# Kernel tuning notes

Measured on AMD Instinct MI355X. Metric: run time of the kernel, lower is better.

## Reference

```python
import jax, jax.numpy as jnp
import numpy as np

H = 1024        # hidden_size
NH = 16         # num_attention_heads
DH = H // NH    # head dim = 64
I = 4096        # intermediate_size
E = 8           # moe_num_experts
B, S = 2, 2048
EPS = 1e-12


def _ln(x, g, b):
    mu = jnp.mean(x, axis=-1, keepdims=True)
    var = jnp.mean(jnp.square(x - mu), axis=-1, keepdims=True)
    return (x - mu) * jax.lax.rsqrt(var + EPS) * g + b


def setup_inputs() -> dict:
    key = jax.random.key(0)
    ks = jax.random.split(key, 16)
    std = 0.02
    p = {
        "hidden_states": jax.random.normal(ks[0], (B, S, H), jnp.float32),
        "Wq": jax.random.normal(ks[1], (H, H), jnp.float32) * std,
        "bq": jnp.zeros((H,), jnp.float32),
        "Wk": jax.random.normal(ks[2], (H, H), jnp.float32) * std,
        "bk": jnp.zeros((H,), jnp.float32),
        "Wv": jax.random.normal(ks[3], (H, H), jnp.float32) * std,
        "bv": jnp.zeros((H,), jnp.float32),
        "Wao": jax.random.normal(ks[4], (H, H), jnp.float32) * std,
        "bao": jnp.zeros((H,), jnp.float32),
        "ln1_g": jnp.ones((H,), jnp.float32),
        "ln1_b": jnp.zeros((H,), jnp.float32),
        "router_w": jax.random.normal(ks[5], (H, E), jnp.float32) * std,
        "We": jax.random.normal(ks[6], (E, H, I), jnp.float32) * std,
        "be": jnp.zeros((E, I), jnp.float32),
        "Wo": jax.random.normal(ks[7], (I, H), jnp.float32) * std,
        "bo": jnp.zeros((H,), jnp.float32),
        "ln2_g": jnp.ones((H,), jnp.float32),
        "ln2_b": jnp.zeros((H,), jnp.float32),
    }
    return p


def reference(hidden_states, Wq, bq, Wk, bk, Wv, bv, Wao, bao, ln1_g, ln1_b,
              router_w, We, be, Wo, bo, ln2_g, ln2_b):
    x = hidden_states  # [B,S,H]

    def heads(t):  # [B,S,H] -> [B,NH,S,DH]
        return t.reshape(B, S, NH, DH).transpose(0, 2, 1, 3)

    q = heads(x @ Wq + bq)
    k = heads(x @ Wk + bk)
    v = heads(x @ Wv + bv)
    scores = jnp.einsum("bhqd,bhkd->bhqk", q, k) / jnp.sqrt(jnp.float32(DH))
    probs = jax.nn.softmax(scores, axis=-1)
    ctx = jnp.einsum("bhqk,bhkd->bhqd", probs, v)
    ctx = ctx.transpose(0, 2, 1, 3).reshape(B, S, H)
    attn_out = _ln(ctx @ Wao + bao + x, ln1_g, ln1_b)  # BertSelfOutput

    # ---- MoE FFN: top-1 routing, per-expert GELU MLP, shared output proj ----
    flat = attn_out.reshape(-1, H)              # [N,H]
    logits = flat @ router_w                    # [N,E]
    idx = jnp.argmax(logits, axis=-1)           # top-1 of softmax == argmax of logits
    inter = jnp.zeros((flat.shape[0], I), flat.dtype)
    for e in range(E):  # small fixed expert count
        h_e = jax.nn.gelu(flat @ We[e] + be[e], approximate=False)
        inter = jnp.where((idx == e)[:, None], h_e, inter)
    inter = inter.reshape(B, S, I)
    out = _ln(inter @ Wo + bo + attn_out, ln2_g, ln2_b)  # BertOutput
    return out
```

## Files before the change

### kernel.cpp

```cpp
#include <hip/hip_runtime.h>
#include <hip/hip_bf16.h>
#include <cstdint>

#define H_  1024
#define NH_ 16
#define DH_ 64
#define I_  4096
#define E_  8
#define B_  2
#define S_  2048
#define N_  4096
#define QKVLD 3072
#define LN_EPS 1e-12f

typedef __attribute__((ext_vector_type(4))) float f4;
typedef __attribute__((ext_vector_type(8))) short s8v;
typedef unsigned int u32;

__device__ __forceinline__ float bf2f(unsigned short u) {
  union { unsigned int i; float f; } c; c.i = ((unsigned int)u) << 16; return c.f;
}
__device__ __forceinline__ unsigned short f2bf(float f) {
  __hip_bfloat16 h = __float2bfloat16(f);
  return *reinterpret_cast<unsigned short*>(&h);
}
__device__ __forceinline__ u32 pack_bf2(float a, float b) {
  return (u32)f2bf(a) | ((u32)f2bf(b) << 16);
}
__device__ __forceinline__ float gelu_f(float x) {
  return 0.5f * x * (1.0f + erff(x * 0.70710678118f));
}
__device__ __forceinline__ void gload16(const void* g, void* l) {
  __builtin_amdgcn_global_load_lds(
      (const __attribute__((address_space(1))) void*)g,
      (__attribute__((address_space(3))) void*)l, 16, 0, 0);
}

__global__ __launch_bounds__(256) void cvt_bf16_kernel(
    const float* __restrict__ in, ushort* __restrict__ out, int n8)
{
  const int t = blockIdx.x * 256 + threadIdx.x;
  if (t >= n8) return;
  const f4 x0 = *(const f4*)(in + (size_t)t * 8);
  const f4 x1 = *(const f4*)(in + (size_t)t * 8 + 4);
  s8v o;
#pragma unroll
  for (int j = 0; j < 4; ++j) { o[j] = (short)f2bf(x0[j]); o[4 + j] = (short)f2bf(x1[j]); }
  *(s8v*)(out + (size_t)t * 8) = o;
}

__global__ __launch_bounds__(256) void transpose_cvt_kernel(
    const float* __restrict__ in, ushort* __restrict__ out, int R, int C)
{
  __shared__ float tile[32][33];
  const size_t zo = (size_t)blockIdx.z * R * C;
  const int bx = blockIdx.x << 5, by = blockIdx.y << 5;
  const int tx = threadIdx.x & 31, ty = threadIdx.x >> 5;
  const float* ip = in + zo + (size_t)by * C + bx;
#pragma unroll
  for (int i = 0; i < 4; ++i)
    tile[ty + 8 * i][tx] = ip[(size_t)(ty + 8 * i) * C + tx];
  __syncthreads();
  ushort* op = out + zo + (size_t)bx * R + by;
#pragma unroll
  for (int i = 0; i < 4; ++i)
    op[(size_t)(ty + 8 * i) * R + tx] = f2bf(tile[tx][ty + 8 * i]);
}

__global__ void concat3_kernel(const float* a, const float* b, const float* c,
                               float* __restrict__ o)
{
  const int t = blockIdx.x * 256 + threadIdx.x;
  if (t < 1024) o[t] = a[t];
  else if (t < 2048) o[t] = b[t - 1024];
  else o[t] = c[t - 2048];
}

__global__ __launch_bounds__(256) void gather_kernel(
    const ushort* __restrict__ X, const int* __restrict__ lists,
    ushort* __restrict__ Xg)
{
  const int r = (blockIdx.x << 1) + (threadIdx.x >> 7);
  const int c = (threadIdx.x & 127) << 3;
  const int tok = lists[r];
  *(s8v*)&Xg[(size_t)r * H_ + c] = *(const s8v*)&X[(size_t)tok * H_ + c];
}

template <bool BF16OUT, int KSPLIT>
__global__ __launch_bounds__(256, 4) void gemm_mfma_kernel(
    const ushort* __restrict__ A, const ushort* __restrict__ Bt,
    const float* __restrict__ bias, void* __restrict__ Cout,
    const int M, const int N, const int K)
{
  __shared__ __align__(16) ushort Asm[2][4][128][8];
  __shared__ __align__(16) ushort Bsm[2][4][128][8];
  const int tid = threadIdx.x;
  const int w = tid >> 6, l = tid & 63;
  const int lq = l & 15, g = l >> 4;
  const int wm = w >> 1, wn = w & 1;
  const int nbx = N >> 7;
  const int nwg = nbx * (M >> 7);
  int id = blockIdx.y * nbx + blockIdx.x;
  id = (id & 7) * (nwg >> 3) + (id >> 3);
  const int m0 = (id / nbx) << 7, n0 = (id % nbx) << 7;
  const int Kspan = K / KSPLIT;
  const int kbase = (KSPLIT > 1) ? blockIdx.z * Kspan : 0;

  const ushort* a0 = A + (size_t)(m0 + l) * K + kbase + (w << 3);
  const ushort* a1 = a0 + (size_t)64 * K;
  const ushort* b0 = Bt + (size_t)(n0 + l) * K + kbase + (w << 3);
  const ushort* b1 = b0 + (size_t)64 * K;

  f4 acc[4][4] = {};
  const int nt = Kspan >> 5;
#define STAGE_G(tt, buf)                                   \
  { const int kt_ = (tt) << 5;                             \
    gload16(a0 + kt_, &Asm[buf][w][0][0]);                 \
    gload16(a1 + kt_, &Asm[buf][w][64][0]);                \
    gload16(b0 + kt_, &Bsm[buf][w][0][0]);                 \
    gload16(b1 + kt_, &Bsm[buf][w][64][0]); }
  STAGE_G(0, 0);
  STAGE_G(1, 1);
  for (int t = 0; t < nt; ++t) {
    const int cur = t & 1;
    if (t + 1 < nt) { asm volatile("s_waitcnt vmcnt(4)" ::: "memory"); }
    else            { asm volatile("s_waitcnt vmcnt(0)" ::: "memory"); }
    __builtin_amdgcn_s_barrier();
    __builtin_amdgcn_sched_barrier(0);
    s8v af[4], bfv[4];
#pragma unroll
    for (int mi = 0; mi < 4; ++mi)
      af[mi] = *(const s8v*)&Asm[cur][g][(wm << 6) + (mi << 4) + lq][0];
#pragma unroll
    for (int ni = 0; ni < 4; ++ni)
      bfv[ni] = *(const s8v*)&Bsm[cur][g][(wn << 6) + (ni << 4) + lq][0];
    asm volatile("s_waitcnt lgkmcnt(0)" ::: "memory");
    __builtin_amdgcn_sched_barrier(0);
    __builtin_amdgcn_s_barrier();
    __builtin_amdgcn_sched_barrier(0);
    if (t + 2 < nt) STAGE_G(t + 2, cur);
#pragma unroll
    for (int mi = 0; mi < 4; ++mi)
#pragma unroll
      for (int ni = 0; ni < 4; ++ni)
        acc[mi][ni] = __builtin_amdgcn_mfma_f32_16x16x32_bf16(af[mi], bfv[ni], acc[mi][ni], 0, 0, 0);
  }
#undef STAGE_G
  if constexpr (BF16OUT) {
    ushort* st = (ushort*)Asm + (size_t)w * (16 * 72);
    float bs[4];
#pragma unroll
    for (int ni = 0; ni < 4; ++ni) bs[ni] = bias[n0 + (wn << 6) + (ni << 4) + lq];
#pragma unroll
    for (int mi = 0; mi < 4; ++mi) {
#pragma unroll
      for (int ni = 0; ni < 4; ++ni)
#pragma unroll
        for (int r = 0; r < 4; ++r)
          st[((g << 2) + r) * 72 + (ni << 4) + lq] = f2bf(acc[mi][ni][r] + bs[ni]);
#pragma unroll
      for (int q2 = 0; q2 < 2; ++q2) {
        const int r16 = l & 15, ch = (l >> 4) + (q2 << 2);
        const s8v vv = *(const s8v*)&st[r16 * 72 + (ch << 3)];
        *(s8v*)&((ushort*)Cout)[(size_t)(m0 + (wm << 6) + (mi << 4) + r16) * N
                                + n0 + (wn << 6) + (ch << 3)] = vv;
      }
    }
  } else {
    float* outf = (float*)Cout + (size_t)blockIdx.z * M * N;
#pragma unroll
    for (int ni = 0; ni < 4; ++ni) {
      const int col = n0 + (wn << 6) + (ni << 4) + lq;
      const float bs = (KSPLIT == 1 || blockIdx.z == 0) ? bias[col] : 0.f;
#pragma unroll
      for (int mi = 0; mi < 4; ++mi) {
        const int row = m0 + (wm << 6) + (mi << 4) + (g << 2);
#pragma unroll
        for (int r = 0; r < 4; ++r)
          outf[(size_t)(row + r) * N + col] = acc[mi][ni][r] + bs;
      }
    }
  }
}

__global__ __launch_bounds__(256, 4) void moe_mfma_kernel(
    const ushort* __restrict__ Xg, const ushort* __restrict__ WeT,
    const float* __restrict__ be, const int* __restrict__ lists,
    const int* __restrict__ offs, const int* __restrict__ cnt,
    const int* __restrict__ tb, ushort* __restrict__ inter)
{
  __shared__ __align__(16) ushort Asm[2][4][128][8];
  __shared__ __align__(16) ushort Bsm[2][4][128][8];
  __shared__ int tokL[128];
  const int by = blockIdx.y;
  if (by >= tb[E_]) return;
  int e = 0;
#pragma unroll
  for (int t = 1; t < E_; ++t) if (by >= tb[t]) e = t;
  const int rt = by - tb[e];
  const int base = offs[e] + (rt << 7);
  const int nrows = cnt[e] - (rt << 7);
  const int tid = threadIdx.x;
  if (tid < 128) tokL[tid] = (tid < nrows) ? lists[base + tid] : -1;
  __syncthreads();
  const int w = tid >> 6, l = tid & 63;
  const int lq = l & 15, g = l >> 4;
  const int wm = w >> 1, wn = w & 1;
  const int n0 = blockIdx.x << 7;
  const int r0 = min(base + l, N_ - 1);
  const int r1 = min(base + 64 + l, N_ - 1);
  const ushort* a0 = Xg + (size_t)r0 * H_ + (w << 3);
  const ushort* a1 = Xg + (size_t)r1 * H_ + (w << 3);
  const ushort* Wp = WeT + (size_t)e * I_ * H_;
  const ushort* b0 = Wp + (size_t)(n0 + l) * H_ + (w << 3);
  const ushort* b1 = b0 + (size_t)64 * H_;

  f4 acc[4][4] = {};
#define STAGE_M(tt, buf)                                   \
  { const int kt_ = (tt) << 5;                             \
    gload16(a0 + kt_, &Asm[buf][w][0][0]);                 \
    gload16(a1 + kt_, &Asm[buf][w][64][0]);                \
    gload16(b0 + kt_, &Bsm[buf][w][0][0]);                 \
    gload16(b1 + kt_, &Bsm[buf][w][64][0]); }
  STAGE_M(0, 0);
  STAGE_M(1, 1);
  for (int t = 0; t < 32; ++t) {
    const int cur = t & 1;
    if (t + 1 < 32) { asm volatile("s_waitcnt vmcnt(4)" ::: "memory"); }
    else            { asm volatile("s_waitcnt vmcnt(0)" ::: "memory"); }
    __builtin_amdgcn_s_barrier();
    __builtin_amdgcn_sched_barrier(0);
    s8v af[4], bfv[4];
#pragma unroll
    for (int mi = 0; mi < 4; ++mi)
      af[mi] = *(const s8v*)&Asm[cur][g][(wm << 6) + (mi << 4) + lq][0];
#pragma unroll
    for (int ni = 0; ni < 4; ++ni)
      bfv[ni] = *(const s8v*)&Bsm[cur][g][(wn << 6) + (ni << 4) + lq][0];
    asm volatile("s_waitcnt lgkmcnt(0)" ::: "memory");
    __builtin_amdgcn_sched_barrier(0);
    __builtin_amdgcn_s_barrier();
    __builtin_amdgcn_sched_barrier(0);
    if (t + 2 < 32) STAGE_M(t + 2, cur);
#pragma unroll
    for (int mi = 0; mi < 4; ++mi)
#pragma unroll
      for (int ni = 0; ni < 4; ++ni)
        acc[mi][ni] = __builtin_amdgcn_mfma_f32_16x16x32_bf16(af[mi], bfv[ni], acc[mi][ni], 0, 0, 0);
  }
#undef STAGE_M
  {
    ushort* st = (ushort*)Asm + (size_t)w * (16 * 72);
    float bs[4];
#pragma unroll
    for (int ni = 0; ni < 4; ++ni) bs[ni] = be[(size_t)e * I_ + n0 + (wn << 6) + (ni << 4) + lq];
#pragma unroll
    for (int mi = 0; mi < 4; ++mi) {
#pragma unroll
      for (int ni = 0; ni < 4; ++ni)
#pragma unroll
        for (int r = 0; r < 4; ++r)
          st[((g << 2) + r) * 72 + (ni << 4) + lq] = f2bf(gelu_f(acc[mi][ni][r] + bs[ni]));
#pragma unroll
      for (int q2 = 0; q2 < 2; ++q2) {
        const int r16 = l & 15, ch = (l >> 4) + (q2 << 2);
        const int tok = tokL[(wm << 6) + (mi << 4) + r16];
        if (tok >= 0) {
          const s8v vv = *(const s8v*)&st[r16 * 72 + (ch << 3)];
          *(s8v*)&inter[(size_t)tok * I_ + n0 + (wn << 6) + (ch << 3)] = vv;
        }
      }
    }
  }
}

__global__ __launch_bounds__(256) void attn_mfma_kernel(
    const ushort* __restrict__ qkv, ushort* __restrict__ ctx)
{
  __shared__ __align__(16) ushort Ks[64 * 72];
  __shared__ __align__(16) ushort Vr[64 * 72];
  __shared__ __align__(16) ushort Vt[64 * 72];
  __shared__ __align__(16) ushort Ps[4][16 * 72];
  const int bid0 = blockIdx.x;
  const int bid  = ((bid0 & 7) << 7) + (bid0 >> 3);
  const int bh = bid >> 5, qt = bid & 31;
  const int b = bh >> 4, h = bh & 15;
  const int tid = threadIdx.x, w = tid >> 6, l = tid & 63;
  const int lq = l & 15, g = l >> 4;
  const size_t bS = (size_t)b * S_;
  const ushort* qb = qkv + bS * QKVLD + h * DH_;
  const ushort* kb = qb + 1024;
  const ushort* vb = qb + 2048;

  s8v qf0, qf1;
  {
    const ushort* qp = qb + (size_t)(qt * 64 + w * 16 + lq) * QKVLD;
    qf0 = *(const s8v*)(qp + (g << 3));
    qf1 = *(const s8v*)(qp + 32 + (g << 3));
  }

  f4 o0 = {0,0,0,0}, o1 = {0,0,0,0}, o2 = {0,0,0,0}, o3 = {0,0,0,0};
  float mrun = -3.0e38f, lrun = 0.f;

  const int skey = tid >> 2;
  const int sd   = (tid & 3) << 4;

  s8v kr0, kr1, vr0, vr1;
#define ALOAD(t_) {                                                        \
    const ushort* kp_ = kb + (size_t)((t_) * 64 + skey) * QKVLD + sd;      \
    kr0 = *(const s8v*)kp_; kr1 = *(const s8v*)(kp_ + 8);                  \
    const ushort* vp_ = vb + (size_t)((t_) * 64 + skey) * QKVLD + sd;      \
    vr0 = *(const s8v*)vp_; vr1 = *(const s8v*)(vp_ + 8); }
#define AWRITE() {                                                         \
    *(s8v*)&Ks[skey * 72 + sd]     = kr0;                                  \
    *(s8v*)&Ks[skey * 72 + sd + 8] = kr1;                                  \
    *(s8v*)&Vr[skey * 72 + sd]     = vr0;                                  \
    *(s8v*)&Vr[skey * 72 + sd + 8] = vr1; }

  ALOAD(0); AWRITE();
  ALOAD(1);

  for (int kt = 0; kt < 32; ++kt) {
    asm volatile("s_waitcnt lgkmcnt(0)" ::: "memory");
    __builtin_amdgcn_sched_barrier(0);
    __builtin_amdgcn_s_barrier();
    __builtin_amdgcn_sched_barrier(0);

    {
      s8v t0, t1;
#pragma unroll
      for (int j = 0; j < 8; ++j) {
        t0[j] = (short)Vr[(w * 16 + j) * 72 + l];
        t1[j] = (short)Vr[(w * 16 + 8 + j) * 72 + l];
      }
      *(s8v*)&Vt[l * 72 + w * 16]     = t0;
      *(s8v*)&Vt[l * 72 + w * 16 + 8] = t1;
    }

    float s[16];
    __builtin_amdgcn_s_setprio(1);
#pragma unroll
    for (int st = 0; st < 4; ++st) {
      f4 acc = {0, 0, 0, 0};
      const s8v ka0 = *(const s8v*)&Ks[(st * 16 + lq) * 72 + (g << 3)];
      const s8v ka1 = *(const s8v*)&Ks[(st * 16 + lq) * 72 + 32 + (g << 3)];
      acc = __builtin_amdgcn_mfma_f32_16x16x32_bf16(ka0, qf0, acc, 0, 0, 0);
      acc = __builtin_amdgcn_mfma_f32_16x16x32_bf16(ka1, qf1, acc, 0, 0, 0);
      s[st * 4 + 0] = acc[0] * 0.125f; s[st * 4 + 1] = acc[1] * 0.125f;
      s[st * 4 + 2] = acc[2] * 0.125f; s[st * 4 + 3] = acc[3] * 0.125f;
    }
    __builtin_amdgcn_s_setprio(0);

    float tmax = s[0];
#pragma unroll
    for (int i = 1; i < 16; ++i) tmax = fmaxf(tmax, s[i]);
    tmax = fmaxf(tmax, __shfl_xor(tmax, 16));
    tmax = fmaxf(tmax, __shfl_xor(tmax, 32));
    if (!__all(tmax - mrun <= 8.f)) {
      const float mnew  = fmaxf(mrun, tmax);
      const float alpha = __expf(mrun - mnew);
      f4 av;
      av[0] = __shfl(alpha, g * 4 + 0); av[1] = __shfl(alpha, g * 4 + 1);
      av[2] = __shfl(alpha, g * 4 + 2); av[3] = __shfl(alpha, g * 4 + 3);
      o0 *= av; o1 *= av; o2 *= av; o3 *= av;
      lrun *= alpha; mrun = mnew;
    }
    float psum = 0.f;
#pragma unroll
    for (int i = 0; i < 16; ++i) { s[i] = __expf(s[i] - mrun); psum += s[i]; }
    psum += __shfl_xor(psum, 16); psum += __shfl_xor(psum, 32);
    lrun += psum;

    {
      ushort* pw = &Ps[w][lq * 72];
#pragma unroll
      for (int st = 0; st < 4; ++st) {
        *(u32*)&pw[st * 16 + g * 4 + 0] = pack_bf2(s[st * 4 + 0], s[st * 4 + 1]);
        *(u32*)&pw[st * 16 + g * 4 + 2] = pack_bf2(s[st * 4 + 2], s[st * 4 + 3]);
      }
    }
    asm volatile("s_waitcnt lgkmcnt(0)" ::: "memory");
    __builtin_amdgcn_sched_barrier(0);
    __builtin_amdgcn_s_barrier();
    __builtin_amdgcn_sched_barrier(0);

    __builtin_amdgcn_s_setprio(1);
#pragma unroll
    for (int ks = 0; ks < 2; ++ks) {
      const int kof = ks * 32 + (g << 3);
      const s8v pa = *(const s8v*)&Ps[w][lq * 72 + kof];
      const s8v v0 = *(const s8v*)&Vt[( 0 + lq) * 72 + kof];
      const s8v v1 = *(const s8v*)&Vt[(16 + lq) * 72 + kof];
      const s8v v2 = *(const s8v*)&Vt[(32 + lq) * 72 + kof];
      const s8v v3 = *(const s8v*)&Vt[(48 + lq) * 72 + kof];
      o0 = __builtin_amdgcn_mfma_f32_16x16x32_bf16(pa, v0, o0, 0, 0, 0);
      o1 = __builtin_amdgcn_mfma_f32_16x16x32_bf16(pa, v1, o1, 0, 0, 0);
      o2 = __builtin_amdgcn_mfma_f32_16x16x32_bf16(pa, v2, o2, 0, 0, 0);
      o3 = __builtin_amdgcn_mfma_f32_16x16x32_bf16(pa, v3, o3, 0, 0, 0);
    }
    __builtin_amdgcn_s_setprio(0);

    if (kt + 1 < 32) AWRITE();
    if (kt + 2 < 32) ALOAD(kt + 2);
  }
#undef ALOAD
#undef AWRITE

  const float inv = 1.f / lrun;
#pragma unroll
  for (int r = 0; r < 4; ++r) {
    const float li = __shfl(inv, g * 4 + r);
    ushort* op = ctx + (bS + (size_t)(qt * 64 + w * 16 + g * 4 + r)) * H_ + h * DH_ + lq;
    op[0]  = f2bf(o0[r] * li);
    op[16] = f2bf(o1[r] * li);
    op[32] = f2bf(o2[r] * li);
    op[48] = f2bf(o3[r] * li);
  }
}

template <int P>
__global__ __launch_bounds__(256) void add_ln_kernel(
    const float* __restrict__ a, const float* __restrict__ r,
    const float* __restrict__ g, const float* __restrict__ bta,
    float* __restrict__ out, ushort* __restrict__ ob)
{
  const int row = blockIdx.x, tid = threadIdx.x;
  const size_t base = (size_t)row * H_;
  const float4 xr = *(const float4*)(r + base + (tid << 2));
  float4 x = xr;
#pragma unroll
  for (int pp = 0; pp < P; ++pp) {
    const float4 xa = *(const float4*)(a + (size_t)pp * N_ * H_ + base + (tid << 2));
    x.x += xa.x; x.y += xa.y; x.z += xa.z; x.w += xa.w;
  }
  float s  = x.x + x.y + x.z + x.w;
  float ss = x.x * x.x + x.y * x.y + x.z * x.z + x.w * x.w;
#pragma unroll
  for (int off = 1; off < 64; off <<= 1) { s += __shfl_xor(s, off); ss += __shfl_xor(ss, off); }
  __shared__ float red[8];
  const int w = tid >> 6, ln = tid & 63;
  if (ln == 0) { red[w] = s; red[4 + w] = ss; }
  __syncthreads();
  const float S  = red[0] + red[1] + red[2] + red[3];
  const float SS = red[4] + red[5] + red[6] + red[7];
  const float mu  = S * (1.f / 1024.f);
  const float var = fmaxf(SS * (1.f / 1024.f) - mu * mu, 0.f);
  const float inv = rsqrtf(var + LN_EPS);
  const float4 gg = *(const float4*)&g[tid << 2];
  const float4 bb = *(const float4*)&bta[tid << 2];
  float4 y;
  y.x = (x.x - mu) * inv * gg.x + bb.x;
  y.y = (x.y - mu) * inv * gg.y + bb.y;
  y.z = (x.z - mu) * inv * gg.z + bb.z;
  y.w = (x.w - mu) * inv * gg.w + bb.w;
  *(float4*)&out[base + (tid << 2)] = y;
  if (ob) {
    ushort4 u;
    u.x = f2bf(y.x); u.y = f2bf(y.y); u.z = f2bf(y.z); u.w = f2bf(y.w);
    *(ushort4*)&ob[base + (tid << 2)] = u;
  }
}

__global__ __launch_bounds__(64) void router_kernel(
    const float* __restrict__ x, const float* __restrict__ rw,
    int* __restrict__ idx, int* __restrict__ cnt)
{
  const int t = blockIdx.x, lane = threadIdx.x;
  float acc[8] = {0.f};
  for (int c = 0; c < H_; c += 64) {
    const float xv = x[(size_t)t * H_ + c + lane];
    const float* wr = rw + (size_t)(c + lane) * E_;
    const float4 w0 = *(const float4*)wr;
    const float4 w1 = *(const float4*)(wr + 4);
    acc[0] += xv * w0.x; acc[1] += xv * w0.y; acc[2] += xv * w0.z; acc[3] += xv * w0.w;
    acc[4] += xv * w1.x; acc[5] += xv * w1.y; acc[6] += xv * w1.z; acc[7] += xv * w1.w;
  }
#pragma unroll
  for (int e = 0; e < E_; ++e) {
    float s = acc[e];
#pragma unroll
    for (int off = 1; off < 64; off <<= 1) s += __shfl_xor(s, off);
    acc[e] = s;
  }
  if (lane == 0) {
    int be_ = 0; float bv = acc[0];
#pragma unroll
    for (int e = 1; e < E_; ++e) if (acc[e] > bv) { bv = acc[e]; be_ = e; }
    idx[t] = be_;
    atomicAdd(&cnt[be_], 1);
  }
}

__global__ void init_kernel(int* cnt) { if (threadIdx.x < E_) cnt[threadIdx.x] = 0; }

__global__ void scan_kernel(const int* __restrict__ cnt, int* __restrict__ offs,
                            int* __restrict__ cursor, int* __restrict__ tb)
{
  int o = 0, tt = 0;
  for (int e = 0; e < E_; ++e) {
    offs[e] = o; cursor[e] = o; tb[e] = tt;
    o += cnt[e]; tt += (cnt[e] + 127) >> 7;
  }
  tb[E_] = tt;
}

__global__ __launch_bounds__(256) void scatter_kernel(
    const int* __restrict__ idx, int* __restrict__ cursor, int* __restrict__ lists)
{
  const int t = blockIdx.x * 256 + threadIdx.x;
  if (t < N_) {
    const int e = idx[t];
    const int p = atomicAdd(&cursor[e], 1);
    lists[p] = t;
  }
}

extern "C" void kernel_launch(void* const* d_in, const int* in_sizes, int n_in,
                              void* d_out, int out_size, void* d_ws, size_t ws_size,
                              hipStream_t stream) {
  const float* x   = (const float*)d_in[0];
  const float* Wq  = (const float*)d_in[1];
  const float* bq  = (const float*)d_in[2];
  const float* Wk  = (const float*)d_in[3];
  const float* bk  = (const float*)d_in[4];
  const float* Wv  = (const float*)d_in[5];
  const float* bv  = (const float*)d_in[6];
  const float* Wao = (const float*)d_in[7];
  const float* bao = (const float*)d_in[8];
  const float* g1  = (const float*)d_in[9];
  const float* b1  = (const float*)d_in[10];
  const float* rw  = (const float*)d_in[11];
  const float* We  = (const float*)d_in[12];
  const float* be  = (const float*)d_in[13];
  const float* Wo  = (const float*)d_in[14];
  const float* bo  = (const float*)d_in[15];
  const float* g2  = (const float*)d_in[16];
  const float* b2  = (const float*)d_in[17];
  float* out = (float*)d_out;

  char* p = (char*)d_ws;
  int* idx    = (int*)p; p += (size_t)N_ * 4;
  int* cnt    = (int*)p; p += 8 * 4;
  int* offs   = (int*)p; p += 8 * 4;
  int* cursor = (int*)p; p += 8 * 4;
  int* tb     = (int*)p; p += 16 * 4;
  int* lists  = (int*)p; p += (size_t)N_ * 4;
  p = (char*)(((uintptr_t)p + 255) & ~(uintptr_t)255);
  const size_t NH = (size_t)N_ * H_;
  ushort* xb     = (ushort*)p; p += NH * 2;
  ushort* qkvb   = (ushort*)p;
  float*  woPart = (float*)p;  p += (size_t)N_ * QKVLD * 2;
  ushort* ctxb   = (ushort*)p; p += NH * 2;
  float*  attn   = (float*)p;  p += NH * 4;
  ushort* attnb  = (ushort*)p; p += NH * 2;
  ushort* interb = (ushort*)p;
  float*  aoPart = (float*)p;  p += (size_t)N_ * I_ * 2;
  ushort* WqkvT  = (ushort*)p; p += (size_t)QKVLD * H_ * 2;
  ushort* WaoT   = (ushort*)p; p += (size_t)H_ * H_ * 2;
  ushort* WoT    = (ushort*)p; p += (size_t)H_ * I_ * 2;
  ushort* WeT    = (ushort*)p; p += (size_t)E_ * I_ * H_ * 2;
  float*  bqkv   = (float*)p;  p += QKVLD * 4;
  ushort* Xg     = xb;

  const dim3 blk(256);

  init_kernel<<<1, 64, 0, stream>>>(cnt);
  cvt_bf16_kernel<<<(N_ * H_ / 8 + 255) / 256, blk, 0, stream>>>(x, xb, N_ * H_ / 8);
  concat3_kernel<<<QKVLD / 256, blk, 0, stream>>>(bq, bk, bv, bqkv);
  transpose_cvt_kernel<<<dim3(32, 32, 1), blk, 0, stream>>>(Wq, WqkvT, H_, H_);
  transpose_cvt_kernel<<<dim3(32, 32, 1), blk, 0, stream>>>(Wk, WqkvT + (size_t)1024 * H_, H_, H_);
  transpose_cvt_kernel<<<dim3(32, 32, 1), blk, 0, stream>>>(Wv, WqkvT + (size_t)2048 * H_, H_, H_);
  transpose_cvt_kernel<<<dim3(32, 32, 1), blk, 0, stream>>>(Wao, WaoT, H_, H_);
  transpose_cvt_kernel<<<dim3(32, 128, 1), blk, 0, stream>>>(Wo, WoT, I_, H_);
  transpose_cvt_kernel<<<dim3(128, 32, 8), blk, 0, stream>>>(We, WeT, H_, I_);

  gemm_mfma_kernel<true, 1><<<dim3(QKVLD / 128, N_ / 128), blk, 0, stream>>>(
      xb, WqkvT, bqkv, qkvb, N_, QKVLD, H_);
  attn_mfma_kernel<<<1024, blk, 0, stream>>>(qkvb, ctxb);
  gemm_mfma_kernel<false, 2><<<dim3(H_ / 128, N_ / 128, 2), blk, 0, stream>>>(
      ctxb, WaoT, bao, aoPart, N_, H_, H_);
  add_ln_kernel<2><<<N_, blk, 0, stream>>>(aoPart, x, g1, b1, attn, attnb);
  router_kernel<<<N_, 64, 0, stream>>>(attn, rw, idx, cnt);
  scan_kernel<<<1, 1, 0, stream>>>(cnt, offs, cursor, tb);
  scatter_kernel<<<N_ / 256, blk, 0, stream>>>(idx, cursor, lists);
  gather_kernel<<<N_ / 2, blk, 0, stream>>>(attnb, lists, Xg);
  moe_mfma_kernel<<<dim3(I_ / 128, N_ / 128 + E_), blk, 0, stream>>>(
      Xg, WeT, be, lists, offs, cnt, tb, interb);
  gemm_mfma_kernel<false, 2><<<dim3(H_ / 128, N_ / 128, 2), blk, 0, stream>>>(
      interb, WoT, bo, woPart, N_, H_, I_);
  add_ln_kernel<2><<<N_, blk, 0, stream>>>(woPart, attn, g2, b2, out, (ushort*)nullptr);
}
```

Before: 506.1 us.

## Use triple-buffered LDS in GEMMs and vectorize the weight transpose-convert kernel

```diff
diff --git a/kernel.cpp b/kernel.cpp
--- a/kernel.cpp
+++ b/kernel.cpp
@@ -52,19 +52,27 @@
 __global__ __launch_bounds__(256) void transpose_cvt_kernel(
     const float* __restrict__ in, ushort* __restrict__ out, int R, int C)
 {
-  __shared__ float tile[32][33];
-  const size_t zo = (size_t)blockIdx.z * R * C;
-  const int bx = blockIdx.x << 5, by = blockIdx.y << 5;
-  const int tx = threadIdx.x & 31, ty = threadIdx.x >> 5;
-  const float* ip = in + zo + (size_t)by * C + bx;
+  __shared__ float Ls[64][68];
+  const size_t zo = (size_t)blockIdx.z * (size_t)R * C;
+  const int bx = blockIdx.x << 6;
+  const int by = blockIdx.y << 6;
+  const int tid = threadIdx.x;
+  const int lr = tid >> 4, lc4 = (tid & 15) << 2;
+  const float* ip = in + zo + (size_t)(by + lr) * C + bx + lc4;
 #pragma unroll
   for (int i = 0; i < 4; ++i)
-    tile[ty + 8 * i][tx] = ip[(size_t)(ty + 8 * i) * C + tx];
+    *(f4*)&Ls[lr + (i << 4)][lc4] = *(const f4*)(ip + (size_t)(i << 4) * C);
   __syncthreads();
-  ushort* op = out + zo + (size_t)bx * R + by;
-#pragma unroll
-  for (int i = 0; i < 4; ++i)
-    op[(size_t)(ty + 8 * i) * R + tx] = f2bf(tile[tx][ty + 8 * i]);
+  const int oc = tid >> 2, seg = (tid & 3) << 4;
+  ushort* op = out + zo + (size_t)(bx + oc) * R + by + seg;
+  s8v v0, v1;
+#pragma unroll
+  for (int j = 0; j < 8; ++j) {
+    v0[j] = (short)f2bf(Ls[seg + j][oc]);
+    v1[j] = (short)f2bf(Ls[seg + 8 + j][oc]);
+  }
+  *(s8v*)op = v0;
+  *(s8v*)(op + 8) = v1;
 }
 
 __global__ void concat3_kernel(const float* a, const float* b, const float* c,
@@ -87,13 +95,13 @@
 }
 
 template <bool BF16OUT, int KSPLIT>
-__global__ __launch_bounds__(256, 4) void gemm_mfma_kernel(
+__global__ __launch_bounds__(256, 3) void gemm_mfma_kernel(
     const ushort* __restrict__ A, const ushort* __restrict__ Bt,
     const float* __restrict__ bias, void* __restrict__ Cout,
     const int M, const int N, const int K)
 {
-  __shared__ __align__(16) ushort Asm[2][4][128][8];
-  __shared__ __align__(16) ushort Bsm[2][4][128][8];
+  __shared__ __align__(16) ushort Asm[3][4][128][8];
+  __shared__ __align__(16) ushort Bsm[3][4][128][8];
   const int tid = threadIdx.x;
   const int w = tid >> 6, l = tid & 63;
   const int lq = l & 15, g = l >> 4;
@@ -121,12 +129,13 @@
     gload16(b1 + kt_, &Bsm[buf][w][64][0]); }
   STAGE_G(0, 0);
   STAGE_G(1, 1);
+  int cur = 0, nxt2 = 2;
   for (int t = 0; t < nt; ++t) {
-    const int cur = t & 1;
     if (t + 1 < nt) { asm volatile("s_waitcnt vmcnt(4)" ::: "memory"); }
     else            { asm volatile("s_waitcnt vmcnt(0)" ::: "memory"); }
     __builtin_amdgcn_s_barrier();
     __builtin_amdgcn_sched_barrier(0);
+    if (t + 2 < nt) STAGE_G(t + 2, nxt2);
     s8v af[4], bfv[4];
 #pragma unroll
     for (int mi = 0; mi < 4; ++mi)
@@ -136,14 +145,13 @@
       bfv[ni] = *(const s8v*)&Bsm[cur][g][(wn << 6) + (ni << 4) + lq][0];
     asm volatile("s_waitcnt lgkmcnt(0)" ::: "memory");
     __builtin_amdgcn_sched_barrier(0);
-    __builtin_amdgcn_s_barrier();
-    __builtin_amdgcn_sched_barrier(0);
-    if (t + 2 < nt) STAGE_G(t + 2, cur);
 #pragma unroll
     for (int mi = 0; mi < 4; ++mi)
 #pragma unroll
       for (int ni = 0; ni < 4; ++ni)
         acc[mi][ni] = __builtin_amdgcn_mfma_f32_16x16x32_bf16(af[mi], bfv[ni], acc[mi][ni], 0, 0, 0);
+    cur = (cur == 2) ? 0 : cur + 1;
+    nxt2 = (nxt2 == 2) ? 0 : nxt2 + 1;
   }
 #undef STAGE_G
   if constexpr (BF16OUT) {
@@ -183,14 +191,14 @@
   }
 }
 
-__global__ __launch_bounds__(256, 4) void moe_mfma_kernel(
+__global__ __launch_bounds__(256, 3) void moe_mfma_kernel(
     const ushort* __restrict__ Xg, const ushort* __restrict__ WeT,
     const float* __restrict__ be, const int* __restrict__ lists,
     const int* __restrict__ offs, const int* __restrict__ cnt,
     const int* __restrict__ tb, ushort* __restrict__ inter)
 {
-  __shared__ __align__(16) ushort Asm[2][4][128][8];
-  __shared__ __align__(16) ushort Bsm[2][4][128][8];
+  __shared__ __align__(16) ushort Asm[3][4][128][8];
+  __shared__ __align__(16) ushort Bsm[3][4][128][8];
   __shared__ int tokL[128];
   const int by = blockIdx.y;
   if (by >= tb[E_]) return;
@@ -224,12 +232,13 @@
     gload16(b1 + kt_, &Bsm[buf][w][64][0]); }
   STAGE_M(0, 0);
   STAGE_M(1, 1);
+  int cur = 0, nxt2 = 2;
   for (int t = 0; t < 32; ++t) {
-    const int cur = t & 1;
     if (t + 1 < 32) { asm volatile("s_waitcnt vmcnt(4)" ::: "memory"); }
     else            { asm volatile("s_waitcnt vmcnt(0)" ::: "memory"); }
     __builtin_amdgcn_s_barrier();
     __builtin_amdgcn_sched_barrier(0);
+    if (t + 2 < 32) STAGE_M(t + 2, nxt2);
     s8v af[4], bfv[4];
 #pragma unroll
     for (int mi = 0; mi < 4; ++mi)
@@ -239,14 +248,13 @@
       bfv[ni] = *(const s8v*)&Bsm[cur][g][(wn << 6) + (ni << 4) + lq][0];
     asm volatile("s_waitcnt lgkmcnt(0)" ::: "memory");
     __builtin_amdgcn_sched_barrier(0);
-    __builtin_amdgcn_s_barrier();
-    __builtin_amdgcn_sched_barrier(0);
-    if (t + 2 < 32) STAGE_M(t + 2, cur);
 #pragma unroll
     for (int mi = 0; mi < 4; ++mi)
 #pragma unroll
       for (int ni = 0; ni < 4; ++ni)
         acc[mi][ni] = __builtin_amdgcn_mfma_f32_16x16x32_bf16(af[mi], bfv[ni], acc[mi][ni], 0, 0, 0);
+    cur = (cur == 2) ? 0 : cur + 1;
+    nxt2 = (nxt2 == 2) ? 0 : nxt2 + 1;
   }
 #undef STAGE_M
   {
@@ -567,12 +575,12 @@
   init_kernel<<<1, 64, 0, stream>>>(cnt);
   cvt_bf16_kernel<<<(N_ * H_ / 8 + 255) / 256, blk, 0, stream>>>(x, xb, N_ * H_ / 8);
   concat3_kernel<<<QKVLD / 256, blk, 0, stream>>>(bq, bk, bv, bqkv);
-  transpose_cvt_kernel<<<dim3(32, 32, 1), blk, 0, stream>>>(Wq, WqkvT, H_, H_);
-  transpose_cvt_kernel<<<dim3(32, 32, 1), blk, 0, stream>>>(Wk, WqkvT + (size_t)1024 * H_, H_, H_);
-  transpose_cvt_kernel<<<dim3(32, 32, 1), blk, 0, stream>>>(Wv, WqkvT + (size_t)2048 * H_, H_, H_);
-  transpose_cvt_kernel<<<dim3(32, 32, 1), blk, 0, stream>>>(Wao, WaoT, H_, H_);
-  transpose_cvt_kernel<<<dim3(32, 128, 1), blk, 0, stream>>>(Wo, WoT, I_, H_);
-  transpose_cvt_kernel<<<dim3(128, 32, 8), blk, 0, stream>>>(We, WeT, H_, I_);
+  transpose_cvt_kernel<<<dim3(16, 16, 1), blk, 0, stream>>>(Wq, WqkvT, H_, H_);
+  transpose_cvt_kernel<<<dim3(16, 16, 1), blk, 0, stream>>>(Wk, WqkvT + (size_t)1024 * H_, H_, H_);
+  transpose_cvt_kernel<<<dim3(16, 16, 1), blk, 0, stream>>>(Wv, WqkvT + (size_t)2048 * H_, H_, H_);
+  transpose_cvt_kernel<<<dim3(16, 16, 1), blk, 0, stream>>>(Wao, WaoT, H_, H_);
+  transpose_cvt_kernel<<<dim3(16, 64, 1), blk, 0, stream>>>(Wo, WoT, I_, H_);
+  transpose_cvt_kernel<<<dim3(64, 16, 8), blk, 0, stream>>>(We, WeT, H_, I_);
 
   gemm_mfma_kernel<true, 1><<<dim3(QKVLD / 128, N_ / 128), blk, 0, stream>>>(
       xb, WqkvT, bqkv, qkvb, N_, QKVLD, H_);
```

Result: no change. 509.8 us (+0.7%).
